# Kernel tuning notes

Hardware: AMD Instinct MI355X
Metric: run time of the kernel (lower is better)

## Reference

```python
import jax, jax.numpy as jnp
import numpy as np

DIM = 1024
CODEBOOK_SIZE = 8192
CODEBOOK_DIM = 16
NUM_CODEBOOKS = 4
BATCH = 4
SEQ = 1024
LN_EPS = 1e-5
COS_EPS = 1e-8  # torch cosine_similarity eps


def setup_inputs() -> dict:
    key = jax.random.key(0)
    k1, k2, k3 = jax.random.split(key, 3)
    x = jax.random.normal(k1, (BATCH, SEQ, DIM), dtype=jnp.float32)
    # xavier_normal_: std = sqrt(2 / (fan_in + fan_out)) over last two dims
    xavier_std = float(np.sqrt(2.0 / (DIM + CODEBOOK_DIM)))
    rand_projs = jax.random.normal(k2, (NUM_CODEBOOKS, DIM, CODEBOOK_DIM), dtype=jnp.float32) * xavier_std
    cb = jax.random.normal(k3, (NUM_CODEBOOKS, CODEBOOK_SIZE, CODEBOOK_DIM), dtype=jnp.float32)
    cb = cb / jnp.clip(jnp.linalg.norm(cb, axis=-1, keepdims=True), 1e-12, None)  # F.normalize
    return {"x": x, "rand_projs": rand_projs, "CB": cb}


def reference(x, rand_projs, CB):
    # LayerNorm(dim, elementwise_affine=False)
    mean = jnp.mean(x, axis=-1, keepdims=True)
    var = jnp.mean(jnp.square(x - mean), axis=-1, keepdims=True)
    xn = (x - mean) * jax.lax.rsqrt(var + LN_EPS)
    # random projection: (b,t,d),(h,d,k) -> (h,b,t,k)
    proj = jnp.einsum('btd,hdk->hbtk', xn, rand_projs)
    # cosine similarity == normalize both then dot (torch clamps norm at eps)
    proj_n = proj / jnp.maximum(jnp.linalg.norm(proj, axis=-1, keepdims=True), COS_EPS)
    cb_n = CB / jnp.maximum(jnp.linalg.norm(CB, axis=-1, keepdims=True), COS_EPS)
    # distances: (h,b,t,cs)  (matches torch stack(h,b,cs,t).permute(0,1,3,2))
    distances = jnp.einsum('hbtk,hck->hbtc', proj_n, cb_n)
    # indices: argmax over codebook, stacked (h,b,t) -> permute(1,2,0) -> (b,t,h)
    indices = jnp.argmax(distances, axis=-1).transpose(1, 2, 0)
    return indices, distances
```

## Files before the change

### kernel.cpp

```cpp
#include <hip/hip_runtime.h>
#include <hip/hip_bf16.h>

#define NH 4
#define BT 4096
#define DD 1024
#define CK 16
#define CS 8192

#define WS_STATS 0
#define WS_PART  8192
#define WS_PROJN 1056768
#define WS_CBN   1318912

__global__ __launch_bounds__(256) void k_stats(const float* __restrict__ x,
                                               float* __restrict__ stats) {
  const int lane = threadIdx.x & 63;
  const int row  = blockIdx.x * 4 + (threadIdx.x >> 6);
  const float4* xr = reinterpret_cast<const float4*>(x + (size_t)row * DD);
  float4 v[4];
  float s = 0.f;
#pragma unroll
  for (int i = 0; i < 4; ++i) {
    v[i] = xr[lane + 64 * i];
    s += (v[i].x + v[i].y) + (v[i].z + v[i].w);
  }
#pragma unroll
  for (int m = 32; m >= 1; m >>= 1) s += __shfl_xor(s, m, 64);
  const float mean = s * (1.f / DD);
  float vs = 0.f;
#pragma unroll
  for (int i = 0; i < 4; ++i) {
    float a = v[i].x - mean, b = v[i].y - mean, c = v[i].z - mean, d = v[i].w - mean;
    vs += (a * a + b * b) + (c * c + d * d);
  }
#pragma unroll
  for (int m = 32; m >= 1; m >>= 1) vs += __shfl_xor(vs, m, 64);
  if (lane == 0) {
    stats[2 * row]     = mean;
    stats[2 * row + 1] = rsqrtf(vs * (1.f / DD) + 1e-5f);
  }
}

__global__ __launch_bounds__(256) void k_proj(const float* __restrict__ x,
                                              const float* __restrict__ stats,
                                              const float* __restrict__ P,
                                              float* __restrict__ part) {
  __shared__ float xa[32][68];
  __shared__ float pa[32][68];
  const int tile = blockIdx.x & 63;
  const int ds   = blockIdx.x >> 6;
  const int tid  = threadIdx.x;
  const int tx = tid & 15, ty = tid >> 4;
  const int r0 = ty * 4, o0 = tx * 4;
  float acc[4][4] = {};

  for (int dc = 0; dc < 256; dc += 32) {
    const int d0 = ds * 256 + dc;
    {
      const int row  = tid >> 2;
      const int rowg = tile * 64 + row;
      const float mean = stats[2 * rowg];
      const float rstd = stats[2 * rowg + 1];
      const float* xp = x + (size_t)rowg * DD + d0 + (tid & 3) * 8;
      float4 a = reinterpret_cast<const float4*>(xp)[0];
      float4 b = reinterpret_cast<const float4*>(xp)[1];
      const int dd = (tid & 3) * 8;
      xa[dd + 0][row] = (a.x - mean) * rstd;
      xa[dd + 1][row] = (a.y - mean) * rstd;
      xa[dd + 2][row] = (a.z - mean) * rstd;
      xa[dd + 3][row] = (a.w - mean) * rstd;
      xa[dd + 4][row] = (b.x - mean) * rstd;
      xa[dd + 5][row] = (b.y - mean) * rstd;
      xa[dd + 6][row] = (b.z - mean) * rstd;
      xa[dd + 7][row] = (b.w - mean) * rstd;
    }
    {
      const int h  = tid >> 6;
      const int f0 = (tid & 63) * 8;
      const float* pp = P + (size_t)h * DD * CK + (size_t)d0 * CK + f0;
      float4 a = reinterpret_cast<const float4*>(pp)[0];
      float4 b = reinterpret_cast<const float4*>(pp)[1];
      float vv[8] = {a.x, a.y, a.z, a.w, b.x, b.y, b.z, b.w};
#pragma unroll
      for (int j = 0; j < 8; ++j) {
        int f = f0 + j;
        pa[f >> 4][(h << 4) | (f & 15)] = vv[j];
      }
    }
    __syncthreads();
#pragma unroll
    for (int d = 0; d < 32; ++d) {
      float4 xv = *reinterpret_cast<const float4*>(&xa[d][r0]);
      float4 pv = *reinterpret_cast<const float4*>(&pa[d][o0]);
      float xr[4] = {xv.x, xv.y, xv.z, xv.w};
      float pr[4] = {pv.x, pv.y, pv.z, pv.w};
#pragma unroll
      for (int i = 0; i < 4; ++i)
#pragma unroll
        for (int j = 0; j < 4; ++j) acc[i][j] = fmaf(xr[i], pr[j], acc[i][j]);
    }
    __syncthreads();
  }
  float* pb = part + ((size_t)ds * BT + tile * 64) * 64;
#pragma unroll
  for (int i = 0; i < 4; ++i) {
    float4 o = {acc[i][0], acc[i][1], acc[i][2], acc[i][3]};
    *reinterpret_cast<float4*>(pb + (size_t)(r0 + i) * 64 + o0) = o;
  }
}

__global__ __launch_bounds__(256) void k_norm(const float* __restrict__ part,
                                              float* __restrict__ proj_n) {
  const int t   = blockIdx.x * 256 + threadIdx.x;
  const int row = t >> 2, h = t & 3;
  float s[16];
#pragma unroll
  for (int k = 0; k < 16; ++k) s[k] = 0.f;
#pragma unroll
  for (int ds = 0; ds < 4; ++ds) {
    const float* pb = part + (size_t)ds * BT * 64 + (size_t)row * 64 + h * 16;
#pragma unroll
    for (int w = 0; w < 4; ++w) {
      float4 v = reinterpret_cast<const float4*>(pb)[w];
      s[w * 4 + 0] += v.x; s[w * 4 + 1] += v.y; s[w * 4 + 2] += v.z; s[w * 4 + 3] += v.w;
    }
  }
  float nsq = 0.f;
#pragma unroll
  for (int k = 0; k < 16; ++k) nsq = fmaf(s[k], s[k], nsq);
  const float inv = 1.f / fmaxf(sqrtf(nsq), 1e-8f);
  float* op = proj_n + ((size_t)h * BT + row) * 16;
#pragma unroll
  for (int w = 0; w < 4; ++w) {
    float4 v = {s[w*4+0] * inv, s[w*4+1] * inv, s[w*4+2] * inv, s[w*4+3] * inv};
    reinterpret_cast<float4*>(op)[w] = v;
  }
}

__global__ __launch_bounds__(256) void k_cbn(const float* __restrict__ CB,
                                             float* __restrict__ cb_n) {
  const int t = blockIdx.x * 256 + threadIdx.x;
  const float4* src = reinterpret_cast<const float4*>(CB + (size_t)t * 16);
  float4 v[4];
  float nsq = 0.f;
#pragma unroll
  for (int w = 0; w < 4; ++w) {
    v[w] = src[w];
    nsq = fmaf(v[w].x, v[w].x, nsq); nsq = fmaf(v[w].y, v[w].y, nsq);
    nsq = fmaf(v[w].z, v[w].z, nsq); nsq = fmaf(v[w].w, v[w].w, nsq);
  }
  const float inv = 1.f / fmaxf(sqrtf(nsq), 1e-8f);
  float4* dst = reinterpret_cast<float4*>(cb_n + (size_t)t * 16);
#pragma unroll
  for (int w = 0; w < 4; ++w) {
    float4 o = {v[w].x * inv, v[w].y * inv, v[w].z * inv, v[w].w * inv};
    dst[w] = o;
  }
}

__global__ __launch_bounds__(256) void k_dist(const float* __restrict__ proj_n,
                                              const float* __restrict__ cb_n,
                                              float* __restrict__ dist,
                                              float* __restrict__ idx_out) {
  __shared__ float q[16][16];
  __shared__ float redv[16][4];
  __shared__ int   redi[16][4];
  const int h    = blockIdx.x >> 8;
  const int tile = blockIdx.x & 255;
  const int tid  = threadIdx.x;

  if (tid < 64) {
    const int r = tid >> 2, k4 = tid & 3;
    float4 v = *reinterpret_cast<const float4*>(
        proj_n + ((size_t)h * BT + tile * 16 + r) * 16 + k4 * 4);
    *reinterpret_cast<float4*>(&q[r][k4 * 4]) = v;
  }
  __syncthreads();

  float best[16];
  int   bidx[16];
#pragma unroll
  for (int r = 0; r < 16; ++r) { best[r] = -2e30f; bidx[r] = 0; }

  const float* cbh = cb_n + (size_t)h * CS * CK;
  float* db = dist + ((size_t)h * BT + tile * 16) * CS;

  for (int cc = 0; cc < 16; ++cc) {
    const int c = cc * 512 + tid * 2;
    float4 cb[2][4];
    const float4* cs = reinterpret_cast<const float4*>(cbh + (size_t)c * CK);
#pragma unroll
    for (int j = 0; j < 2; ++j)
#pragma unroll
      for (int w = 0; w < 4; ++w) cb[j][w] = cs[j * 4 + w];

#pragma unroll
    for (int r = 0; r < 16; ++r) {
      float4 q0 = *reinterpret_cast<const float4*>(&q[r][0]);
      float4 q1 = *reinterpret_cast<const float4*>(&q[r][4]);
      float4 q2 = *reinterpret_cast<const float4*>(&q[r][8]);
      float4 q3 = *reinterpret_cast<const float4*>(&q[r][12]);
      float dj[2];
#pragma unroll
      for (int j = 0; j < 2; ++j) {
        float s =        cb[j][0].x * q0.x;
        s = fmaf(cb[j][0].y, q0.y, s);
        s = fmaf(cb[j][0].z, q0.z, s);
        s = fmaf(cb[j][0].w, q0.w, s);
        s = fmaf(cb[j][1].x, q1.x, s);
        s = fmaf(cb[j][1].y, q1.y, s);
        s = fmaf(cb[j][1].z, q1.z, s);
        s = fmaf(cb[j][1].w, q1.w, s);
        s = fmaf(cb[j][2].x, q2.x, s);
        s = fmaf(cb[j][2].y, q2.y, s);
        s = fmaf(cb[j][2].z, q2.z, s);
        s = fmaf(cb[j][2].w, q2.w, s);
        s = fmaf(cb[j][3].x, q3.x, s);
        s = fmaf(cb[j][3].y, q3.y, s);
        s = fmaf(cb[j][3].z, q3.z, s);
        s = fmaf(cb[j][3].w, q3.w, s);
        dj[j] = s;
      }
      float2 dots = {dj[0], dj[1]};
      *reinterpret_cast<float2*>(db + (size_t)r * CS + c) = dots;
#pragma unroll
      for (int j = 0; j < 2; ++j) {
        if (dj[j] > best[r]) { best[r] = dj[j]; bidx[r] = c + j; }
      }
      __builtin_amdgcn_sched_barrier(0);
    }
  }

  const int lane = tid & 63, wv = tid >> 6;
#pragma unroll
  for (int r = 0; r < 16; ++r) {
    float v = best[r];
    int   ii = bidx[r];
#pragma unroll
    for (int m = 32; m >= 1; m >>= 1) {
      float ov = __shfl_xor(v, m, 64);
      int   oi = __shfl_xor(ii, m, 64);
      if (ov > v || (ov == v && oi < ii)) { v = ov; ii = oi; }
    }
    if (lane == 0) { redv[r][wv] = v; redi[r][wv] = ii; }
  }
  __syncthreads();
  if (tid < 16) {
    const int r = tid;
    float v = redv[r][0];
    int   ii = redi[r][0];
#pragma unroll
    for (int w = 1; w < 4; ++w) {
      float ov = redv[r][w];
      int   oi = redi[r][w];
      if (ov > v || (ov == v && oi < ii)) { v = ov; ii = oi; }
    }
    const int rowg = tile * 16 + r;
    idx_out[(size_t)rowg * 4 + h] = (float)ii;
  }
}

extern "C" void kernel_launch(void* const* d_in, const int* in_sizes, int n_in,
                              void* d_out, int out_size, void* d_ws, size_t ws_size,
                              hipStream_t stream) {
  (void)in_sizes; (void)n_in; (void)out_size; (void)ws_size;
  const float* x  = (const float*)d_in[0];
  const float* P  = (const float*)d_in[1];
  const float* CB = (const float*)d_in[2];
  float* ws  = (float*)d_ws;
  float* out = (float*)d_out;
  float* idx_out = out;
  float* dist    = out + BT * NH;

  k_stats<<<1024, 256, 0, stream>>>(x, ws + WS_STATS);
  k_proj <<<256,  256, 0, stream>>>(x, ws + WS_STATS, P, ws + WS_PART);
  k_norm <<<64,   256, 0, stream>>>(ws + WS_PART, ws + WS_PROJN);
  k_cbn  <<<128,  256, 0, stream>>>(CB, ws + WS_CBN);
  k_dist <<<1024, 256, 0, stream>>>(ws + WS_PROJN, ws + WS_CBN, dist, idx_out);
}
```

Before: 161.3 us.

## Give each wavefront its own query rows and scan the full codebook per wave

Restructures the distance kernel so each 64-lane wave owns 4 query rows, held in scalar registers via readfirstlane, and walks the entire codebook itself. This removes the shared-memory query tile, the LDS reads of the queries, and the cross-wave argmax reduction with its block barriers. The codebook is now read four times per block, once per wave, instead of once. Fewer rows per thread also means less reuse of each loaded codebook entry. The large distance-store stream is unchanged.

```diff
diff --git a/kernel.cpp b/kernel.cpp
--- a/kernel.cpp
+++ b/kernel.cpp
@@ -158,82 +158,75 @@
   }
 }
 
+__device__ __forceinline__ float dot16(const float q[16], const float4 c[4]) {
+  float s = q[0] * c[0].x;
+  s = fmaf(q[1],  c[0].y, s);
+  s = fmaf(q[2],  c[0].z, s);
+  s = fmaf(q[3],  c[0].w, s);
+  s = fmaf(q[4],  c[1].x, s);
+  s = fmaf(q[5],  c[1].y, s);
+  s = fmaf(q[6],  c[1].z, s);
+  s = fmaf(q[7],  c[1].w, s);
+  s = fmaf(q[8],  c[2].x, s);
+  s = fmaf(q[9],  c[2].y, s);
+  s = fmaf(q[10], c[2].z, s);
+  s = fmaf(q[11], c[2].w, s);
+  s = fmaf(q[12], c[3].x, s);
+  s = fmaf(q[13], c[3].y, s);
+  s = fmaf(q[14], c[3].z, s);
+  s = fmaf(q[15], c[3].w, s);
+  return s;
+}
+
 __global__ __launch_bounds__(256) void k_dist(const float* __restrict__ proj_n,
                                               const float* __restrict__ cb_n,
                                               float* __restrict__ dist,
                                               float* __restrict__ idx_out) {
-  __shared__ float q[16][16];
-  __shared__ float redv[16][4];
-  __shared__ int   redi[16][4];
   const int h    = blockIdx.x >> 8;
   const int tile = blockIdx.x & 255;
-  const int tid  = threadIdx.x;
-
-  if (tid < 64) {
-    const int r = tid >> 2, k4 = tid & 3;
-    float4 v = *reinterpret_cast<const float4*>(
-        proj_n + ((size_t)h * BT + tile * 16 + r) * 16 + k4 * 4);
-    *reinterpret_cast<float4*>(&q[r][k4 * 4]) = v;
-  }
-  __syncthreads();
-
-  float best[16];
-  int   bidx[16];
-#pragma unroll
-  for (int r = 0; r < 16; ++r) { best[r] = -2e30f; bidx[r] = 0; }
+  const int lane = threadIdx.x & 63;
+  const int wv   = __builtin_amdgcn_readfirstlane(threadIdx.x >> 6);
+  const int row0 = tile * 16 + wv * 4;
+
+  float sq[4][16];
+#pragma unroll
+  for (int r = 0; r < 4; ++r) {
+    const float* qp = proj_n + ((size_t)h * BT + row0 + r) * 16;
+#pragma unroll
+    for (int k = 0; k < 16; ++k) {
+      sq[r][k] = __int_as_float(
+          __builtin_amdgcn_readfirstlane(__float_as_int(qp[k])));
+    }
+  }
 
   const float* cbh = cb_n + (size_t)h * CS * CK;
-  float* db = dist + ((size_t)h * BT + tile * 16) * CS;
-
-  for (int cc = 0; cc < 16; ++cc) {
-    const int c = cc * 512 + tid * 2;
-    float4 cb[2][4];
-    const float4* cs = reinterpret_cast<const float4*>(cbh + (size_t)c * CK);
-#pragma unroll
-    for (int j = 0; j < 2; ++j)
-#pragma unroll
-      for (int w = 0; w < 4; ++w) cb[j][w] = cs[j * 4 + w];
-
-#pragma unroll
-    for (int r = 0; r < 16; ++r) {
-      float4 q0 = *reinterpret_cast<const float4*>(&q[r][0]);
-      float4 q1 = *reinterpret_cast<const float4*>(&q[r][4]);
-      float4 q2 = *reinterpret_cast<const float4*>(&q[r][8]);
-      float4 q3 = *reinterpret_cast<const float4*>(&q[r][12]);
-      float dj[2];
-#pragma unroll
-      for (int j = 0; j < 2; ++j) {
-        float s =        cb[j][0].x * q0.x;
-        s = fmaf(cb[j][0].y, q0.y, s);
-        s = fmaf(cb[j][0].z, q0.z, s);
-        s = fmaf(cb[j][0].w, q0.w, s);
-        s = fmaf(cb[j][1].x, q1.x, s);
-        s = fmaf(cb[j][1].y, q1.y, s);
-        s = fmaf(cb[j][1].z, q1.z, s);
-        s = fmaf(cb[j][1].w, q1.w, s);
-        s = fmaf(cb[j][2].x, q2.x, s);
-        s = fmaf(cb[j][2].y, q2.y, s);
-        s = fmaf(cb[j][2].z, q2.z, s);
-        s = fmaf(cb[j][2].w, q2.w, s);
-        s = fmaf(cb[j][3].x, q3.x, s);
-        s = fmaf(cb[j][3].y, q3.y, s);
-        s = fmaf(cb[j][3].z, q3.z, s);
-        s = fmaf(cb[j][3].w, q3.w, s);
-        dj[j] = s;
-      }
-      float2 dots = {dj[0], dj[1]};
-      *reinterpret_cast<float2*>(db + (size_t)r * CS + c) = dots;
-#pragma unroll
-      for (int j = 0; j < 2; ++j) {
-        if (dj[j] > best[r]) { best[r] = dj[j]; bidx[r] = c + j; }
-      }
-      __builtin_amdgcn_sched_barrier(0);
-    }
-  }
-
-  const int lane = tid & 63, wv = tid >> 6;
-#pragma unroll
-  for (int r = 0; r < 16; ++r) {
+  float* db = dist + ((size_t)h * BT + row0) * CS;
+
+  float best[4];
+  int   bidx[4];
+#pragma unroll
+  for (int r = 0; r < 4; ++r) { best[r] = -2e30f; bidx[r] = 0; }
+
+  for (int ch = 0; ch < 64; ++ch) {
+    const int c0 = ch * 128 + lane * 2;
+    const float4* cs = reinterpret_cast<const float4*>(cbh + (size_t)c0 * CK);
+    float4 ca[4], cb[4];
+#pragma unroll
+    for (int w = 0; w < 4; ++w) { ca[w] = cs[w]; cb[w] = cs[4 + w]; }
+
+#pragma unroll
+    for (int r = 0; r < 4; ++r) {
+      float s0 = dot16(sq[r], ca);
+      float s1 = dot16(sq[r], cb);
+      float2 o = {s0, s1};
+      *reinterpret_cast<float2*>(db + (size_t)r * CS + c0) = o;
+      if (s0 > best[r]) { best[r] = s0; bidx[r] = c0; }
+      if (s1 > best[r]) { best[r] = s1; bidx[r] = c0 + 1; }
+    }
+  }
+
+#pragma unroll
+  for (int r = 0; r < 4; ++r) {
     float v = best[r];
     int   ii = bidx[r];
 #pragma unroll
@@ -242,21 +235,9 @@
       int   oi = __shfl_xor(ii, m, 64);
       if (ov > v || (ov == v && oi < ii)) { v = ov; ii = oi; }
     }
-    if (lane == 0) { redv[r][wv] = v; redi[r][wv] = ii; }
-  }
-  __syncthreads();
-  if (tid < 16) {
-    const int r = tid;
-    float v = redv[r][0];
-    int   ii = redi[r][0];
-#pragma unroll
-    for (int w = 1; w < 4; ++w) {
-      float ov = redv[r][w];
-      int   oi = redi[r][w];
-      if (ov > v || (ov == v && oi < ii)) { v = ov; ii = oi; }
-    }
-    const int rowg = tile * 16 + r;
-    idx_out[(size_t)rowg * 4 + h] = (float)ii;
+    if (lane == 0) {
+      idx_out[(size_t)(row0 + r) * 4 + h] = (float)ii;
+    }
   }
 }
 
```

After: 299.0 us. 1.85x slower.
